# Performance work log

Measured on AMD Instinct MI355X. Metric: run time of the kernel, lower is better.

Reference implementation:

```python
import jax, jax.numpy as jnp
import numpy as np

B, S = 256, 16384
HUBER_DELTA = 1.0  # torch.nn.HuberLoss default


def setup_inputs() -> dict:
    key = jax.random.key(0)
    k1, k2, k3 = jax.random.split(key, 3)
    pred_coords = jax.random.normal(k1, (B, S, 3), dtype=jnp.float32)
    target_coords = jax.random.normal(k2, (B, S, 3), dtype=jnp.float32)
    mask = jax.random.randint(k3, (B, S), 0, 2).astype(jnp.int32)
    return {"pred_coords": pred_coords, "target_coords": target_coords, "mask": mask}


def _kabsch_align(pred, target, maskf):
    # pred/target: [B,S,3], maskf: [B,S] (0/1). Batched masked Kabsch.
    cnt = maskf.sum(axis=1, keepdims=True)                      # [B,1]
    cp = (pred * maskf[..., None]).sum(axis=1) / cnt            # [B,3] pred center
    ct = (target * maskf[..., None]).sum(axis=1) / cnt          # [B,3] target center
    pc = (pred - cp[:, None, :]) * maskf[..., None]             # masked centered pred
    tc = target - ct[:, None, :]                                # centered target
    H = jnp.einsum('bsi,bsj->bij', pc, tc)                      # [B,3,3] covariance
    U, _, Vt = jnp.linalg.svd(H)                                # batched 3x3 SVD
    R = jnp.einsum('bji,bkj->bik', Vt, U)                       # Vt^T @ U^T
    sign = jnp.where(jnp.linalg.det(R) < 0, -1.0, 1.0)          # [B] reflection fix
    flip = jnp.ones((pred.shape[0], 3), dtype=pred.dtype).at[:, -1].set(sign)
    Vt = Vt * flip[:, :, None]                                  # flip last row of Vt
    R = jnp.einsum('bji,bkj->bik', Vt, U)
    t = ct - jnp.einsum('bij,bj->bi', R, cp)                    # [B,3]
    aligned = jnp.einsum('bij,bsj->bsi', R, pred) + t[:, None, :]
    return aligned


def _huber(d):
    a = jnp.abs(d)
    return jnp.where(a < HUBER_DELTA, 0.5 * d * d, HUBER_DELTA * (a - 0.5 * HUBER_DELTA))


def reference(pred_coords, target_coords, mask):
    maskf = mask.astype(pred_coords.dtype)                      # [B,S]
    aligned = _kabsch_align(pred_coords, target_coords, maskf)  # [B,S,3]
    # (torch computes a clamped coord_diff here but never uses it in the loss)
    loss = _huber(aligned - target_coords) * maskf[..., None]   # [B,S,3]
    return loss.sum() / maskf.sum()
```

## Files before the change

### kernel.cpp

```cpp
#include <hip/hip_runtime.h>


#define NB 256
#define NS 16384
#define TPB 256
#define PPT 4
#define CHUNKS (NS / (TPB * PPT))
#define NBLK (NB * CHUNKS)

__device__ __forceinline__ float wave_sum(float v) {
#pragma unroll
    for (int o = 32; o > 0; o >>= 1) v += __shfl_xor(v, o, 64);
    return v;
}

__device__ __forceinline__ float huber(float d) {
    float a = fabsf(d);
    return a < 1.f ? 0.5f * d * d : a - 0.5f;
}

__global__ __launch_bounds__(TPB, 8) void reduce_kernel(
    const float* __restrict__ pred, const float* __restrict__ tgt,
    const int* __restrict__ mask, float* __restrict__ part)
{
    const int b = blockIdx.y, j = blockIdx.x, tid = threadIdx.x;
    const long base = (long)b * NS + (long)(j * TPB + tid) * PPT;
    const float4* p4 = reinterpret_cast<const float4*>(pred + base * 3);
    const float4* t4 = reinterpret_cast<const float4*>(tgt + base * 3);
    const float4 pA = p4[0], pB = p4[1], pC = p4[2];
    const float4 tA = t4[0], tB = t4[1], tC = t4[2];
    const int4 m4 = *reinterpret_cast<const int4*>(mask + base);
    float P[4][3] = {{pA.x,pA.y,pA.z},{pA.w,pB.x,pB.y},{pB.z,pB.w,pC.x},{pC.y,pC.z,pC.w}};
    float T[4][3] = {{tA.x,tA.y,tA.z},{tA.w,tB.x,tB.y},{tB.z,tB.w,tC.x},{tC.y,tC.z,tC.w}};
    float m[4] = {(float)m4.x,(float)m4.y,(float)m4.z,(float)m4.w};

    float acc[16];
#pragma unroll
    for (int i = 0; i < 16; ++i) acc[i] = 0.f;
#pragma unroll
    for (int k = 0; k < PPT; ++k) {
        const float mk = m[k];
        const float mp0 = mk * P[k][0], mp1 = mk * P[k][1], mp2 = mk * P[k][2];
        acc[0] += mk;
        acc[1] += mp0;            acc[2] += mp1;            acc[3] += mp2;
        acc[4] += mk * T[k][0];   acc[5] += mk * T[k][1];   acc[6] += mk * T[k][2];
        acc[7]  += mp0 * T[k][0]; acc[8]  += mp0 * T[k][1]; acc[9]  += mp0 * T[k][2];
        acc[10] += mp1 * T[k][0]; acc[11] += mp1 * T[k][1]; acc[12] += mp1 * T[k][2];
        acc[13] += mp2 * T[k][0]; acc[14] += mp2 * T[k][1]; acc[15] += mp2 * T[k][2];
    }
#pragma unroll
    for (int i = 0; i < 16; ++i) acc[i] = wave_sum(acc[i]);

    __shared__ float red[4][16];
    const int wave = tid >> 6, lane = tid & 63;
    if (lane == 0) {
#pragma unroll
        for (int i = 0; i < 16; ++i) red[wave][i] = acc[i];
    }
    __syncthreads();
    if (tid < 16)
        part[((b * CHUNKS + j) << 4) + tid] =
            red[0][tid] + red[1][tid] + red[2][tid] + red[3][tid];
}

__global__ __launch_bounds__(NB) void svd_kernel(
    const float* __restrict__ part, float* __restrict__ RT)
{
    const int b = threadIdx.x;
    const float4* p4 = reinterpret_cast<const float4*>(part);
    float a[16];
#pragma unroll
    for (int i = 0; i < 16; ++i) a[i] = 0.f;
#pragma unroll
    for (int k = 0; k < CHUNKS; ++k) {
        const int row = (b * CHUNKS + k) << 2;
        float4 v0 = p4[row], v1 = p4[row+1], v2 = p4[row+2], v3 = p4[row+3];
        a[0]+=v0.x;  a[1]+=v0.y;  a[2]+=v0.z;  a[3]+=v0.w;
        a[4]+=v1.x;  a[5]+=v1.y;  a[6]+=v1.z;  a[7]+=v1.w;
        a[8]+=v2.x;  a[9]+=v2.y;  a[10]+=v2.z; a[11]+=v2.w;
        a[12]+=v3.x; a[13]+=v3.y; a[14]+=v3.z; a[15]+=v3.w;
    }
    const float cnt = a[0];
    const float inv = 1.f / cnt;
    const float cpx=a[1]*inv, cpy=a[2]*inv, cpz=a[3]*inv;
    const float ctx=a[4]*inv, cty=a[5]*inv, ctz=a[6]*inv;
    const float Sxx = a[7]  - cnt*cpx*ctx;
    const float Sxy = a[8]  - cnt*cpx*cty;
    const float Sxz = a[9]  - cnt*cpx*ctz;
    const float Syx = a[10] - cnt*cpy*ctx;
    const float Syy = a[11] - cnt*cpy*cty;
    const float Syz = a[12] - cnt*cpy*ctz;
    const float Szx = a[13] - cnt*cpz*ctx;
    const float Szy = a[14] - cnt*cpz*cty;
    const float Szz = a[15] - cnt*cpz*ctz;
    float N00 =  Sxx + Syy + Szz;
    float N01 =  Syz - Szy;
    float N02 =  Szx - Sxz;
    float N03 =  Sxy - Syx;
    float N11 =  Sxx - Syy - Szz;
    float N12 =  Sxy + Syx;
    float N13 =  Szx + Sxz;
    float N22 = -Sxx + Syy - Szz;
    float N23 =  Syz + Szy;
    float N33 = -Sxx - Syy + Szz;
    const float fro = sqrtf(N00*N00 + N11*N11 + N22*N22 + N33*N33 +
                2.f*(N01*N01 + N02*N02 + N03*N03 + N12*N12 + N13*N13 + N23*N23));
    const float isc = 1.f / (fro + 1e-30f);
    N00*=isc; N01*=isc; N02*=isc; N03*=isc; N11*=isc;
    N12*=isc; N13*=isc; N22*=isc; N23*=isc; N33*=isc;

    float qw = 1.f, qx = 0.1f, qy = 0.2f, qz = 0.3f;
    for (int it = 0; it < 96; ++it) {
        float nw = N00*qw + N01*qx + N02*qy + N03*qz + qw;
        float nx = N01*qw + N11*qx + N12*qy + N13*qz + qx;
        float ny = N02*qw + N12*qx + N22*qy + N23*qz + qy;
        float nz = N03*qw + N13*qx + N23*qy + N33*qz + qz;
        if ((it & 7) == 7) {
            const float r = rsqrtf(nw*nw + nx*nx + ny*ny + nz*nz);
            nw *= r; nx *= r; ny *= r; nz *= r;
        }
        qw = nw; qx = nx; qy = ny; qz = nz;
    }
    const float r = rsqrtf(qw*qw + qx*qx + qy*qy + qz*qz);
    qw *= r; qx *= r; qy *= r; qz *= r;
    const float R00 = 1.f - 2.f*(qy*qy + qz*qz);
    const float R01 = 2.f*(qx*qy - qw*qz);
    const float R02 = 2.f*(qx*qz + qw*qy);
    const float R10 = 2.f*(qx*qy + qw*qz);
    const float R11 = 1.f - 2.f*(qx*qx + qz*qz);
    const float R12 = 2.f*(qy*qz - qw*qx);
    const float R20 = 2.f*(qx*qz - qw*qy);
    const float R21 = 2.f*(qy*qz + qw*qx);
    const float R22 = 1.f - 2.f*(qx*qx + qy*qy);
    float* o = RT + b * 16;
    o[0]=R00; o[1]=R01; o[2]=R02; o[3]=R10; o[4]=R11; o[5]=R12;
    o[6]=R20; o[7]=R21; o[8]=R22;
    o[9]  = ctx - (R00*cpx + R01*cpy + R02*cpz);
    o[10] = cty - (R10*cpx + R11*cpy + R12*cpz);
    o[11] = ctz - (R20*cpx + R21*cpy + R22*cpz);
    o[12] = cnt;
}

__global__ __launch_bounds__(TPB, 8) void loss_kernel(
    const float* __restrict__ pred, const float* __restrict__ tgt,
    const int* __restrict__ mask, const float* __restrict__ RT,
    float* __restrict__ lpart)
{
    const int b = blockIdx.y, j = blockIdx.x, tid = threadIdx.x;
    __shared__ float C[12];
    if (tid < 12) C[tid] = RT[b * 16 + tid];
    __syncthreads();
    const long base = (long)b * NS + (long)(j * TPB + tid) * PPT;
    const float4* p4 = reinterpret_cast<const float4*>(pred + base * 3);
    const float4* t4 = reinterpret_cast<const float4*>(tgt + base * 3);
    const float4 pA = p4[0], pB = p4[1], pC = p4[2];
    const float4 tA = t4[0], tB = t4[1], tC = t4[2];
    const int4 m4 = *reinterpret_cast<const int4*>(mask + base);
    float P[4][3] = {{pA.x,pA.y,pA.z},{pA.w,pB.x,pB.y},{pB.z,pB.w,pC.x},{pC.y,pC.z,pC.w}};
    float T[4][3] = {{tA.x,tA.y,tA.z},{tA.w,tB.x,tB.y},{tB.z,tB.w,tC.x},{tC.y,tC.z,tC.w}};
    float m[4] = {(float)m4.x,(float)m4.y,(float)m4.z,(float)m4.w};

    float ls = 0.f;
#pragma unroll
    for (int k = 0; k < PPT; ++k) {
        const float ax = C[0]*P[k][0] + C[1]*P[k][1] + C[2]*P[k][2] + C[9];
        const float ay = C[3]*P[k][0] + C[4]*P[k][1] + C[5]*P[k][2] + C[10];
        const float az = C[6]*P[k][0] + C[7]*P[k][1] + C[8]*P[k][2] + C[11];
        ls += m[k] * (huber(ax - T[k][0]) + huber(ay - T[k][1]) + huber(az - T[k][2]));
    }
    ls = wave_sum(ls);
    __shared__ float red[4];
    const int wave = tid >> 6, lane = tid & 63;
    if (lane == 0) red[wave] = ls;
    __syncthreads();
    if (tid == 0) lpart[b * CHUNKS + j] = red[0] + red[1] + red[2] + red[3];
}

__global__ __launch_bounds__(NB) void final_kernel(
    const float* __restrict__ lpart, const float* __restrict__ RT,
    float* __restrict__ out)
{
    const int tid = threadIdx.x;
    float ls = 0.f;
#pragma unroll
    for (int k = 0; k < CHUNKS; ++k) ls += lpart[tid + NB * k];
    float cs = RT[tid * 16 + 12];
    ls = wave_sum(ls);
    cs = wave_sum(cs);
    __shared__ float rl[4], rc[4];
    const int wave = tid >> 6, lane = tid & 63;
    if (lane == 0) { rl[wave] = ls; rc[wave] = cs; }
    __syncthreads();
    if (tid == 0)
        out[0] = (rl[0]+rl[1]+rl[2]+rl[3]) / (rc[0]+rc[1]+rc[2]+rc[3]);
}

extern "C" void kernel_launch(void* const* d_in, const int* in_sizes, int n_in,
                              void* d_out, int out_size, void* d_ws, size_t ws_size,
                              hipStream_t stream) {
    const float* pred = (const float*)d_in[0];
    const float* tgt  = (const float*)d_in[1];
    const int*   mask = (const int*)d_in[2];
    float* out = (float*)d_out;

    float* part  = (float*)d_ws;
    float* RT    = part + NBLK * 16;
    float* lpart = RT + NB * 16;

    dim3 grid(CHUNKS, NB);
    reduce_kernel<<<grid, TPB, 0, stream>>>(pred, tgt, mask, part);
    svd_kernel<<<1, NB, 0, stream>>>(part, RT);
    loss_kernel<<<grid, TPB, 0, stream>>>(pred, tgt, mask, RT, lpart);
    final_kernel<<<1, NB, 0, stream>>>(lpart, RT, out);
}
```

Baseline: 169.2 us.

## Fuse reduction, rotation solve and loss into one per-batch kernel with register caching

Replaces the reduce, svd, and loss kernels with a single kernel where one 512-thread block handles an entire batch row. Each thread keeps 32 points in registers so inputs are read from memory once instead of twice. Block-level reduction feeds a single-thread quaternion eigen solve, and the loss is computed from the cached registers. This risks heavy register pressure, low occupancy (one block per batch), strided per-thread loads, and a serialized solve while other threads idle.

Result: faster. 165.1 us (-2.5%).

```diff
diff --git a/kernel.cpp b/kernel.cpp
--- a/kernel.cpp
+++ b/kernel.cpp
@@ -3,10 +3,9 @@
 
 #define NB 256
 #define NS 16384
-#define TPB 256
-#define PPT 4
-#define CHUNKS (NS / (TPB * PPT))
-#define NBLK (NB * CHUNKS)
+#define TPB 512
+#define PPT 32
+#define NW (TPB / 64)
 
 __device__ __forceinline__ float wave_sum(float v) {
 #pragma unroll
@@ -19,172 +18,166 @@
     return a < 1.f ? 0.5f * d * d : a - 0.5f;
 }
 
-__global__ __launch_bounds__(TPB, 8) void reduce_kernel(
+__global__ __launch_bounds__(TPB, 2) void fused_kernel(
     const float* __restrict__ pred, const float* __restrict__ tgt,
-    const int* __restrict__ mask, float* __restrict__ part)
+    const int* __restrict__ mask,
+    float* __restrict__ bl, float* __restrict__ bc)
 {
-    const int b = blockIdx.y, j = blockIdx.x, tid = threadIdx.x;
-    const long base = (long)b * NS + (long)(j * TPB + tid) * PPT;
+    const int b = blockIdx.x, tid = threadIdx.x;
+    const long base = (long)b * NS + (long)tid * PPT;
     const float4* p4 = reinterpret_cast<const float4*>(pred + base * 3);
     const float4* t4 = reinterpret_cast<const float4*>(tgt + base * 3);
-    const float4 pA = p4[0], pB = p4[1], pC = p4[2];
-    const float4 tA = t4[0], tB = t4[1], tC = t4[2];
-    const int4 m4 = *reinterpret_cast<const int4*>(mask + base);
-    float P[4][3] = {{pA.x,pA.y,pA.z},{pA.w,pB.x,pB.y},{pB.z,pB.w,pC.x},{pC.y,pC.z,pC.w}};
-    float T[4][3] = {{tA.x,tA.y,tA.z},{tA.w,tB.x,tB.y},{tB.z,tB.w,tC.x},{tC.y,tC.z,tC.w}};
-    float m[4] = {(float)m4.x,(float)m4.y,(float)m4.z,(float)m4.w};
+    const int4*   m4 = reinterpret_cast<const int4*>(mask + base);
+
+    float Px[PPT], Py[PPT], Pz[PPT], Tx[PPT], Ty[PPT], Tz[PPT];
+    unsigned int mbits = 0u;
 
     float acc[16];
 #pragma unroll
     for (int i = 0; i < 16; ++i) acc[i] = 0.f;
-#pragma unroll
-    for (int k = 0; k < PPT; ++k) {
-        const float mk = m[k];
-        const float mp0 = mk * P[k][0], mp1 = mk * P[k][1], mp2 = mk * P[k][2];
-        acc[0] += mk;
-        acc[1] += mp0;            acc[2] += mp1;            acc[3] += mp2;
-        acc[4] += mk * T[k][0];   acc[5] += mk * T[k][1];   acc[6] += mk * T[k][2];
-        acc[7]  += mp0 * T[k][0]; acc[8]  += mp0 * T[k][1]; acc[9]  += mp0 * T[k][2];
-        acc[10] += mp1 * T[k][0]; acc[11] += mp1 * T[k][1]; acc[12] += mp1 * T[k][2];
-        acc[13] += mp2 * T[k][0]; acc[14] += mp2 * T[k][1]; acc[15] += mp2 * T[k][2];
-    }
+
+#pragma unroll
+    for (int g = 0; g < PPT / 4; ++g) {
+        const float4 pA = p4[3*g], pB = p4[3*g+1], pC = p4[3*g+2];
+        const float4 tA = t4[3*g], tB = t4[3*g+1], tC = t4[3*g+2];
+        const int4 mm = m4[g];
+        const float P[4][3] = {{pA.x,pA.y,pA.z},{pA.w,pB.x,pB.y},
+                               {pB.z,pB.w,pC.x},{pC.y,pC.z,pC.w}};
+        const float T[4][3] = {{tA.x,tA.y,tA.z},{tA.w,tB.x,tB.y},
+                               {tB.z,tB.w,tC.x},{tC.y,tC.z,tC.w}};
+        const int mi[4] = {mm.x, mm.y, mm.z, mm.w};
+#pragma unroll
+        for (int k = 0; k < 4; ++k) {
+            const int idx = g * 4 + k;
+            const float mk = mi[k] ? 1.f : 0.f;
+            mbits |= (mi[k] ? 1u : 0u) << idx;
+            const float px = mk * P[k][0], py = mk * P[k][1], pz = mk * P[k][2];
+            const float tx = mk * T[k][0], ty = mk * T[k][1], tz = mk * T[k][2];
+            Px[idx] = px; Py[idx] = py; Pz[idx] = pz;
+            Tx[idx] = tx; Ty[idx] = ty; Tz[idx] = tz;
+            acc[0] += mk;
+            acc[1] += px;  acc[2] += py;  acc[3] += pz;
+            acc[4] += tx;  acc[5] += ty;  acc[6] += tz;
+            acc[7]  += px * tx; acc[8]  += px * ty; acc[9]  += px * tz;
+            acc[10] += py * tx; acc[11] += py * ty; acc[12] += py * tz;
+            acc[13] += pz * tx; acc[14] += pz * ty; acc[15] += pz * tz;
+        }
+    }
+
 #pragma unroll
     for (int i = 0; i < 16; ++i) acc[i] = wave_sum(acc[i]);
 
-    __shared__ float red[4][16];
+    __shared__ float red[NW][16];
+    __shared__ float Ssum[16];
+    __shared__ float C[13];
     const int wave = tid >> 6, lane = tid & 63;
     if (lane == 0) {
 #pragma unroll
         for (int i = 0; i < 16; ++i) red[wave][i] = acc[i];
     }
     __syncthreads();
-    if (tid < 16)
-        part[((b * CHUNKS + j) << 4) + tid] =
-            red[0][tid] + red[1][tid] + red[2][tid] + red[3][tid];
-}
-
-__global__ __launch_bounds__(NB) void svd_kernel(
-    const float* __restrict__ part, float* __restrict__ RT)
-{
-    const int b = threadIdx.x;
-    const float4* p4 = reinterpret_cast<const float4*>(part);
-    float a[16];
-#pragma unroll
-    for (int i = 0; i < 16; ++i) a[i] = 0.f;
-#pragma unroll
-    for (int k = 0; k < CHUNKS; ++k) {
-        const int row = (b * CHUNKS + k) << 2;
-        float4 v0 = p4[row], v1 = p4[row+1], v2 = p4[row+2], v3 = p4[row+3];
-        a[0]+=v0.x;  a[1]+=v0.y;  a[2]+=v0.z;  a[3]+=v0.w;
-        a[4]+=v1.x;  a[5]+=v1.y;  a[6]+=v1.z;  a[7]+=v1.w;
-        a[8]+=v2.x;  a[9]+=v2.y;  a[10]+=v2.z; a[11]+=v2.w;
-        a[12]+=v3.x; a[13]+=v3.y; a[14]+=v3.z; a[15]+=v3.w;
-    }
-    const float cnt = a[0];
-    const float inv = 1.f / cnt;
-    const float cpx=a[1]*inv, cpy=a[2]*inv, cpz=a[3]*inv;
-    const float ctx=a[4]*inv, cty=a[5]*inv, ctz=a[6]*inv;
-    const float Sxx = a[7]  - cnt*cpx*ctx;
-    const float Sxy = a[8]  - cnt*cpx*cty;
-    const float Sxz = a[9]  - cnt*cpx*ctz;
-    const float Syx = a[10] - cnt*cpy*ctx;
-    const float Syy = a[11] - cnt*cpy*cty;
-    const float Syz = a[12] - cnt*cpy*ctz;
-    const float Szx = a[13] - cnt*cpz*ctx;
-    const float Szy = a[14] - cnt*cpz*cty;
-    const float Szz = a[15] - cnt*cpz*ctz;
-    float N00 =  Sxx + Syy + Szz;
-    float N01 =  Syz - Szy;
-    float N02 =  Szx - Sxz;
-    float N03 =  Sxy - Syx;
-    float N11 =  Sxx - Syy - Szz;
-    float N12 =  Sxy + Syx;
-    float N13 =  Szx + Sxz;
-    float N22 = -Sxx + Syy - Szz;
-    float N23 =  Syz + Szy;
-    float N33 = -Sxx - Syy + Szz;
-    const float fro = sqrtf(N00*N00 + N11*N11 + N22*N22 + N33*N33 +
-                2.f*(N01*N01 + N02*N02 + N03*N03 + N12*N12 + N13*N13 + N23*N23));
-    const float isc = 1.f / (fro + 1e-30f);
-    N00*=isc; N01*=isc; N02*=isc; N03*=isc; N11*=isc;
-    N12*=isc; N13*=isc; N22*=isc; N23*=isc; N33*=isc;
-
-    float qw = 1.f, qx = 0.1f, qy = 0.2f, qz = 0.3f;
-    for (int it = 0; it < 96; ++it) {
-        float nw = N00*qw + N01*qx + N02*qy + N03*qz + qw;
-        float nx = N01*qw + N11*qx + N12*qy + N13*qz + qx;
-        float ny = N02*qw + N12*qx + N22*qy + N23*qz + qy;
-        float nz = N03*qw + N13*qx + N23*qy + N33*qz + qz;
-        if ((it & 7) == 7) {
-            const float r = rsqrtf(nw*nw + nx*nx + ny*ny + nz*nz);
-            nw *= r; nx *= r; ny *= r; nz *= r;
+    if (tid < 16) {
+        float s = 0.f;
+#pragma unroll
+        for (int w = 0; w < NW; ++w) s += red[w][tid];
+        Ssum[tid] = s;
+    }
+    __syncthreads();
+
+    if (tid == 0) {
+        const float cnt = Ssum[0];
+        const float inv = 1.f / cnt;
+        const float cpx = Ssum[1]*inv, cpy = Ssum[2]*inv, cpz = Ssum[3]*inv;
+        const float ctx = Ssum[4]*inv, cty = Ssum[5]*inv, ctz = Ssum[6]*inv;
+        const float Sxx = Ssum[7]  - cnt*cpx*ctx;
+        const float Sxy = Ssum[8]  - cnt*cpx*cty;
+        const float Sxz = Ssum[9]  - cnt*cpx*ctz;
+        const float Syx = Ssum[10] - cnt*cpy*ctx;
+        const float Syy = Ssum[11] - cnt*cpy*cty;
+        const float Syz = Ssum[12] - cnt*cpy*ctz;
+        const float Szx = Ssum[13] - cnt*cpz*ctx;
+        const float Szy = Ssum[14] - cnt*cpz*cty;
+        const float Szz = Ssum[15] - cnt*cpz*ctz;
+        float N00 =  Sxx + Syy + Szz;
+        float N01 =  Syz - Szy;
+        float N02 =  Szx - Sxz;
+        float N03 =  Sxy - Syx;
+        float N11 =  Sxx - Syy - Szz;
+        float N12 =  Sxy + Syx;
+        float N13 =  Szx + Sxz;
+        float N22 = -Sxx + Syy - Szz;
+        float N23 =  Syz + Szy;
+        float N33 = -Sxx - Syy + Szz;
+        const float fro = sqrtf(N00*N00 + N11*N11 + N22*N22 + N33*N33 +
+              2.f*(N01*N01 + N02*N02 + N03*N03 + N12*N12 + N13*N13 + N23*N23));
+        const float isc = 1.f / (fro + 1e-30f);
+        N00*=isc; N01*=isc; N02*=isc; N03*=isc; N11*=isc;
+        N12*=isc; N13*=isc; N22*=isc; N23*=isc; N33*=isc;
+
+        float qw = 1.f, qx = 0.1f, qy = 0.2f, qz = 0.3f;
+        for (int it = 0; it < 96; ++it) {
+            float nw = N00*qw + N01*qx + N02*qy + N03*qz + qw;
+            float nx = N01*qw + N11*qx + N12*qy + N13*qz + qx;
+            float ny = N02*qw + N12*qx + N22*qy + N23*qz + qy;
+            float nz = N03*qw + N13*qx + N23*qy + N33*qz + qz;
+            if ((it & 7) == 7) {
+                const float r = rsqrtf(nw*nw + nx*nx + ny*ny + nz*nz);
+                nw *= r; nx *= r; ny *= r; nz *= r;
+            }
+            qw = nw; qx = nx; qy = ny; qz = nz;
         }
-        qw = nw; qx = nx; qy = ny; qz = nz;
-    }
-    const float r = rsqrtf(qw*qw + qx*qx + qy*qy + qz*qz);
-    qw *= r; qx *= r; qy *= r; qz *= r;
-    const float R00 = 1.f - 2.f*(qy*qy + qz*qz);
-    const float R01 = 2.f*(qx*qy - qw*qz);
-    const float R02 = 2.f*(qx*qz + qw*qy);
-    const float R10 = 2.f*(qx*qy + qw*qz);
-    const float R11 = 1.f - 2.f*(qx*qx + qz*qz);
-    const float R12 = 2.f*(qy*qz - qw*qx);
-    const float R20 = 2.f*(qx*qz - qw*qy);
-    const float R21 = 2.f*(qy*qz + qw*qx);
-    const float R22 = 1.f - 2.f*(qx*qx + qy*qy);
-    float* o = RT + b * 16;
-    o[0]=R00; o[1]=R01; o[2]=R02; o[3]=R10; o[4]=R11; o[5]=R12;
-    o[6]=R20; o[7]=R21; o[8]=R22;
-    o[9]  = ctx - (R00*cpx + R01*cpy + R02*cpz);
-    o[10] = cty - (R10*cpx + R11*cpy + R12*cpz);
-    o[11] = ctz - (R20*cpx + R21*cpy + R22*cpz);
-    o[12] = cnt;
-}
-
-__global__ __launch_bounds__(TPB, 8) void loss_kernel(
-    const float* __restrict__ pred, const float* __restrict__ tgt,
-    const int* __restrict__ mask, const float* __restrict__ RT,
-    float* __restrict__ lpart)
-{
-    const int b = blockIdx.y, j = blockIdx.x, tid = threadIdx.x;
-    __shared__ float C[12];
-    if (tid < 12) C[tid] = RT[b * 16 + tid];
-    __syncthreads();
-    const long base = (long)b * NS + (long)(j * TPB + tid) * PPT;
-    const float4* p4 = reinterpret_cast<const float4*>(pred + base * 3);
-    const float4* t4 = reinterpret_cast<const float4*>(tgt + base * 3);
-    const float4 pA = p4[0], pB = p4[1], pC = p4[2];
-    const float4 tA = t4[0], tB = t4[1], tC = t4[2];
-    const int4 m4 = *reinterpret_cast<const int4*>(mask + base);
-    float P[4][3] = {{pA.x,pA.y,pA.z},{pA.w,pB.x,pB.y},{pB.z,pB.w,pC.x},{pC.y,pC.z,pC.w}};
-    float T[4][3] = {{tA.x,tA.y,tA.z},{tA.w,tB.x,tB.y},{tB.z,tB.w,tC.x},{tC.y,tC.z,tC.w}};
-    float m[4] = {(float)m4.x,(float)m4.y,(float)m4.z,(float)m4.w};
-
+        const float r = rsqrtf(qw*qw + qx*qx + qy*qy + qz*qz);
+        qw *= r; qx *= r; qy *= r; qz *= r;
+        const float R00 = 1.f - 2.f*(qy*qy + qz*qz);
+        const float R01 = 2.f*(qx*qy - qw*qz);
+        const float R02 = 2.f*(qx*qz + qw*qy);
+        const float R10 = 2.f*(qx*qy + qw*qz);
+        const float R11 = 1.f - 2.f*(qx*qx + qz*qz);
+        const float R12 = 2.f*(qy*qz - qw*qx);
+        const float R20 = 2.f*(qx*qz - qw*qy);
+        const float R21 = 2.f*(qy*qz + qw*qx);
+        const float R22 = 1.f - 2.f*(qx*qx + qy*qy);
+        C[0]=R00; C[1]=R01; C[2]=R02;
+        C[3]=R10; C[4]=R11; C[5]=R12;
+        C[6]=R20; C[7]=R21; C[8]=R22;
+        C[9]  = ctx - (R00*cpx + R01*cpy + R02*cpz);
+        C[10] = cty - (R10*cpx + R11*cpy + R12*cpz);
+        C[11] = ctz - (R20*cpx + R21*cpy + R22*cpz);
+        C[12] = cnt;
+    }
+    __syncthreads();
+
+    const float C0=C[0], C1=C[1], C2=C[2], C3=C[3], C4=C[4],  C5=C[5];
+    const float C6=C[6], C7=C[7], C8=C[8], C9=C[9], C10=C[10], C11=C[11];
     float ls = 0.f;
 #pragma unroll
     for (int k = 0; k < PPT; ++k) {
-        const float ax = C[0]*P[k][0] + C[1]*P[k][1] + C[2]*P[k][2] + C[9];
-        const float ay = C[3]*P[k][0] + C[4]*P[k][1] + C[5]*P[k][2] + C[10];
-        const float az = C[6]*P[k][0] + C[7]*P[k][1] + C[8]*P[k][2] + C[11];
-        ls += m[k] * (huber(ax - T[k][0]) + huber(ay - T[k][1]) + huber(az - T[k][2]));
+        const float mk = (float)((mbits >> k) & 1u);
+        const float ax = C0*Px[k] + C1*Py[k] + C2*Pz[k] + C9;
+        const float ay = C3*Px[k] + C4*Py[k] + C5*Pz[k] + C10;
+        const float az = C6*Px[k] + C7*Py[k] + C8*Pz[k] + C11;
+        ls += mk * (huber(ax - Tx[k]) + huber(ay - Ty[k]) + huber(az - Tz[k]));
     }
     ls = wave_sum(ls);
-    __shared__ float red[4];
-    const int wave = tid >> 6, lane = tid & 63;
-    if (lane == 0) red[wave] = ls;
-    __syncthreads();
-    if (tid == 0) lpart[b * CHUNKS + j] = red[0] + red[1] + red[2] + red[3];
+    __shared__ float redl[NW];
+    if (lane == 0) redl[wave] = ls;
+    __syncthreads();
+    if (tid == 0) {
+        float t = 0.f;
+#pragma unroll
+        for (int w = 0; w < NW; ++w) t += redl[w];
+        bl[b] = t;
+        bc[b] = C[12];
+    }
 }
 
 __global__ __launch_bounds__(NB) void final_kernel(
-    const float* __restrict__ lpart, const float* __restrict__ RT,
+    const float* __restrict__ bl, const float* __restrict__ bc,
     float* __restrict__ out)
 {
     const int tid = threadIdx.x;
-    float ls = 0.f;
-#pragma unroll
-    for (int k = 0; k < CHUNKS; ++k) ls += lpart[tid + NB * k];
-    float cs = RT[tid * 16 + 12];
+    float ls = bl[tid];
+    float cs = bc[tid];
     ls = wave_sum(ls);
     cs = wave_sum(cs);
     __shared__ float rl[4], rc[4];
@@ -203,13 +196,9 @@
     const int*   mask = (const int*)d_in[2];
     float* out = (float*)d_out;
 
-    float* part  = (float*)d_ws;
-    float* RT    = part + NBLK * 16;
-    float* lpart = RT + NB * 16;
-
-    dim3 grid(CHUNKS, NB);
-    reduce_kernel<<<grid, TPB, 0, stream>>>(pred, tgt, mask, part);
-    svd_kernel<<<1, NB, 0, stream>>>(part, RT);
-    loss_kernel<<<grid, TPB, 0, stream>>>(pred, tgt, mask, RT, lpart);
-    final_kernel<<<1, NB, 0, stream>>>(lpart, RT, out);
-}
+    float* bl = (float*)d_ws;
+    float* bc = bl + NB;
+
+    fused_kernel<<<NB, TPB, 0, stream>>>(pred, tgt, mask, bl, bc);
+    final_kernel<<<1, NB, 0, stream>>>(bl, bc, out);
+}
```
